# Performance work log

Hardware: AMD Instinct MI355X
Metric: run time of the kernel (lower is better)

## Reference

```python
import jax, jax.numpy as jnp
import numpy as np

D_MODEL = 768
N_HEADS = 12
D_K = D_MODEL // N_HEADS
NEG = -1e9


def setup_inputs() -> dict:
    key = jax.random.key(0)
    ks = jax.random.split(key, 10)
    B, S = 2, 2048
    x = jax.random.normal(ks[0], (B, S, D_MODEL), dtype=jnp.float32)
    # causal mask, broadcastable over batch and heads
    mask = jnp.tril(jnp.ones((S, S), dtype=jnp.int32))[None, None]
    scale = 1.0 / np.sqrt(D_MODEL)
    def lin(k):
        return jax.random.normal(k, (D_MODEL, D_MODEL), dtype=jnp.float32) * scale
    return {
        "x": x, "mask": mask,
        "wq": lin(ks[1]), "bq": jnp.zeros((D_MODEL,), jnp.float32),
        "wk": lin(ks[2]), "bk": jnp.zeros((D_MODEL,), jnp.float32),
        "wv": lin(ks[3]), "bv": jnp.zeros((D_MODEL,), jnp.float32),
        "wo": lin(ks[4]), "bo": jnp.zeros((D_MODEL,), jnp.float32),
    }


def reference(x, mask, wq, bq, wk, bk, wv, bv, wo, bo):
    B, S, _ = x.shape
    def split_heads(t):  # [B,S,D] -> [B,H,S,dk]
        return t.reshape(B, S, N_HEADS, D_K).transpose(0, 2, 1, 3)
    q = split_heads(x @ wq + bq)
    k = split_heads(x @ wk + bk)
    v = split_heads(x @ wv + bv)
    scores = jnp.einsum("bhqd,bhkd->bhqk", q, k) / jnp.sqrt(jnp.float32(D_K))
    scores = jnp.where(mask == 0, NEG, scores)
    attn = jax.nn.softmax(scores, axis=-1)
    # dropout is identity in eval mode
    ctx = jnp.einsum("bhqk,bhkd->bhqd", attn, v)
    ctx = ctx.transpose(0, 2, 1, 3).reshape(B, S, D_MODEL)
    return ctx @ wo + bo
```

## Files before the change

### kernel.cpp

```cpp
#include <hip/hip_runtime.h>
#include <hip/hip_bf16.h>
#include <stdint.h>

#define DM   768
#define NH   12
#define DKH  64
#define BB   2
#define SS   2048
#define MT   (BB*SS)
#define NQKV (3*DM)

typedef __attribute__((ext_vector_type(8))) short short8;
typedef __attribute__((ext_vector_type(4))) float f32x4;

__device__ __forceinline__ unsigned short f2bf(float f) {
    union { float f; unsigned u; } v; v.f = f;
    unsigned r = v.u + 0x7fffu + ((v.u >> 16) & 1u);
    return (unsigned short)(r >> 16);
}

__device__ __forceinline__ void gload_lds16(const unsigned short* g, unsigned short* l) {
    __builtin_amdgcn_global_load_lds((const __attribute__((address_space(1))) void*)g,
                                     (__attribute__((address_space(3))) void*)l, 16, 0, 0);
}

__global__ void k_conv_x(const float* __restrict__ x, unsigned short* __restrict__ xb) {
    int i = blockIdx.x * 256 + threadIdx.x;
    const float4 v = ((const float4*)x)[i];
    ushort4 o;
    o.x = f2bf(v.x); o.y = f2bf(v.y); o.z = f2bf(v.z); o.w = f2bf(v.w);
    ((ushort4*)xb)[i] = o;
}

__global__ void k_conv_w(const float* __restrict__ wq, const float* __restrict__ wk,
                         const float* __restrict__ wv, const float* __restrict__ wo,
                         unsigned short* __restrict__ wT) {
    __shared__ float tile[32][33];
    const int sel = blockIdx.z;
    const float* w = (sel == 0) ? wq : (sel == 1) ? wk : (sel == 2) ? wv : wo;
    const int k0 = blockIdx.x * 32, n0 = blockIdx.y * 32;
    const int tx = threadIdx.x, ty = threadIdx.y;
    #pragma unroll
    for (int j = 0; j < 4; j++)
        tile[ty + 8*j][tx] = w[(size_t)(k0 + ty + 8*j) * DM + n0 + tx];
    __syncthreads();
    #pragma unroll
    for (int j = 0; j < 4; j++)
        wT[(size_t)(sel*DM + n0 + ty + 8*j) * DM + k0 + tx] = f2bf(tile[tx][ty + 8*j]);
}

__launch_bounds__(256)
__global__ void k_gemm_qkv(const unsigned short* __restrict__ xb,
                           const unsigned short* __restrict__ wT,
                           const float* __restrict__ bq, const float* __restrict__ bk,
                           const float* __restrict__ bv,
                           unsigned short* __restrict__ Qb,
                           unsigned short* __restrict__ Kb,
                           unsigned short* __restrict__ Vt) {
    __shared__ __align__(16) unsigned short As[128][32];
    __shared__ __align__(16) unsigned short Bs[128][32];
    const int t = threadIdx.x;
    const int m0 = blockIdx.x * 128;
    const int n0 = blockIdx.y * 128;
    const int wid = t >> 6, lane = t & 63, q4 = lane >> 4, l16 = lane & 15;
    const int wm = (wid >> 1) * 64, wn = (wid & 1) * 64;

    const int srow = wid * 32 + (lane >> 2);
    const int koff = (lane & 3) * 8;
    const unsigned short* AgL = xb + (size_t)(m0 + srow) * DM + koff;
    const unsigned short* AgH = AgL + (size_t)16 * DM;
    const unsigned short* BgL = wT + (size_t)(n0 + srow) * DM + koff;
    const unsigned short* BgH = BgL + (size_t)16 * DM;
    unsigned short* ldsA1 = &As[wid*32][0];
    unsigned short* ldsA2 = &As[wid*32 + 16][0];
    unsigned short* ldsB1 = &Bs[wid*32][0];
    unsigned short* ldsB2 = &Bs[wid*32 + 16][0];

    f32x4 acc[4][4];
    for (int i = 0; i < 4; i++) for (int j = 0; j < 4; j++)
        acc[i][j] = (f32x4){0.f, 0.f, 0.f, 0.f};

    for (int kt = 0; kt < DM; kt += 32) {
        gload_lds16(AgL + kt, ldsA1);
        gload_lds16(AgH + kt, ldsA2);
        gload_lds16(BgL + kt, ldsB1);
        gload_lds16(BgH + kt, ldsB2);
        __syncthreads();
        short8 af[4], bf[4];
        for (int i = 0; i < 4; i++) af[i] = *(const short8*)&As[wm + i*16 + l16][q4*8];
        for (int i = 0; i < 4; i++) bf[i] = *(const short8*)&Bs[wn + i*16 + l16][q4*8];
        for (int mi = 0; mi < 4; mi++)
            for (int ni = 0; ni < 4; ni++)
                acc[mi][ni] = __builtin_amdgcn_mfma_f32_16x16x32_bf16(af[mi], bf[ni], acc[mi][ni], 0, 0, 0);
        __syncthreads();
    }

    const int sel = n0 / DM;
    const float* bias = (sel == 0) ? bq : (sel == 1) ? bk : bv;
    for (int ni = 0; ni < 4; ni++) {
        const int col = n0 + wn + ni*16 + l16;
        const int c = col - sel * DM;
        const float bsv = bias[c];
        const int h = c >> 6, d = c & 63;
        for (int mi = 0; mi < 4; mi++) {
            for (int r = 0; r < 4; r++) {
                const int row = m0 + wm + mi*16 + q4*4 + r;
                const int b = row >> 11, s = row & 2047;
                const int bh = b * NH + h;
                float v = acc[mi][ni][r] + bsv;
                if (sel == 0) {
                    Qb[(bh*SS + s)*DKH + d] = f2bf(v * 0.125f);
                } else if (sel == 1) {
                    Kb[(bh*SS + s)*DKH + d] = f2bf(v);
                } else {
                    Vt[(bh*DKH + d)*SS + s] = f2bf(v);
                }
            }
        }
    }
}

__launch_bounds__(256)
__global__ void k_attn(const unsigned short* __restrict__ Qb,
                       const unsigned short* __restrict__ Kb,
                       const unsigned short* __restrict__ Vt,
                       unsigned short* __restrict__ ctx) {
    __shared__ __align__(16) unsigned short Ks[2][64][72];
    __shared__ __align__(16) unsigned short Vs[2][64][72];
    __shared__ __align__(16) unsigned short P[4][16][68];
    const int t = threadIdx.x;
    const int wid = t >> 6, lane = t & 63, q4 = lane >> 4, l16 = lane & 15;
    const int lin = blockIdx.x;
    const int bh = lin % (BB * NH);
    const int qblk = 31 - lin / (BB * NH);
    const int b = bh / NH, h = bh - b * NH;
    const int qw = qblk * 64 + wid * 16;

    const unsigned short* Qp = Qb + (size_t)bh * SS * DKH;
    const unsigned short* Kp = Kb + (size_t)bh * SS * DKH;
    const unsigned short* Vp = Vt + (size_t)bh * DKH * SS;

    const int sr = t >> 3;
    const int sc = (t & 7) * 8;

    short8 qf[2];
    for (int kc = 0; kc < 2; kc++)
        qf[kc] = *(const short8*)(Qp + (qw + l16)*DKH + kc*32 + q4*8);

    f32x4 accO[4];
    for (int j = 0; j < 4; j++) accO[j] = (f32x4){0.f, 0.f, 0.f, 0.f};
    float lacc[4] = {0.f, 0.f, 0.f, 0.f};

    {
        uint4 k0 = *(const uint4*)(Kp + (size_t)(sr)      * DKH + sc);
        uint4 k1 = *(const uint4*)(Kp + (size_t)(sr + 32) * DKH + sc);
        uint4 v0 = *(const uint4*)(Vp + (size_t)(sr)      * SS  + sc);
        uint4 v1 = *(const uint4*)(Vp + (size_t)(sr + 32) * SS  + sc);
        *(uint4*)&Ks[0][sr][sc]      = k0;
        *(uint4*)&Ks[0][sr + 32][sc] = k1;
        *(uint4*)&Vs[0][sr][sc]      = v0;
        *(uint4*)&Vs[0][sr + 32][sc] = v1;
    }
    __syncthreads();

    for (int kt = 0; kt <= qblk; kt++) {
        const int cb = kt & 1, nb = cb ^ 1;
        const bool hasN = (kt < qblk);
        uint4 nk0, nk1, nv0, nv1;
        if (hasN) {
            const int kn = (kt + 1) * 64;
            nk0 = *(const uint4*)(Kp + (size_t)(kn + sr)      * DKH + sc);
            nk1 = *(const uint4*)(Kp + (size_t)(kn + sr + 32) * DKH + sc);
            nv0 = *(const uint4*)(Vp + (size_t)(sr)      * SS + kn + sc);
            nv1 = *(const uint4*)(Vp + (size_t)(sr + 32) * SS + kn + sc);
        }
        short8 kf[4][2];
        #pragma unroll
        for (int ni = 0; ni < 4; ni++)
            #pragma unroll
            for (int kc = 0; kc < 2; kc++)
                kf[ni][kc] = *(const short8*)&Ks[cb][ni*16 + l16][kc*32 + q4*8];
        f32x4 S[4];
        #pragma unroll
        for (int j = 0; j < 4; j++) S[j] = (f32x4){0.f, 0.f, 0.f, 0.f};
        #pragma unroll
        for (int ni = 0; ni < 4; ni++) {
            S[ni] = __builtin_amdgcn_mfma_f32_16x16x32_bf16(qf[0], kf[ni][0], S[ni], 0, 0, 0);
            S[ni] = __builtin_amdgcn_mfma_f32_16x16x32_bf16(qf[1], kf[ni][1], S[ni], 0, 0, 0);
        }
        if (kt == qblk) {
            #pragma unroll
            for (int ni = 0; ni < 4; ni++) {
                const int pr = q4*4, pc = ni*16 + l16;
                if (ni > wid) {
                    P[wid][pr+0][pc] = 0; P[wid][pr+1][pc] = 0;
                    P[wid][pr+2][pc] = 0; P[wid][pr+3][pc] = 0;
                    continue;
                }
                float p[4];
                if (ni == wid) {
                    #pragma unroll
                    for (int r = 0; r < 4; r++) {
                        const int qrow = qw + q4*4 + r;
                        const int key = qblk*64 + ni*16 + l16;
                        p[r] = (key > qrow) ? 0.f : __expf(S[ni][r]);
                        lacc[r] += p[r];
                    }
                } else {
                    #pragma unroll
                    for (int r = 0; r < 4; r++) {
                        p[r] = __expf(S[ni][r]);
                        lacc[r] += p[r];
                    }
                }
                union { __hip_bfloat162 v; unsigned u; } u01, u23;
                u01.v = __float22bfloat162_rn(make_float2(p[0], p[1]));
                u23.v = __float22bfloat162_rn(make_float2(p[2], p[3]));
                P[wid][pr+0][pc] = (unsigned short)(u01.u & 0xffffu);
                P[wid][pr+1][pc] = (unsigned short)(u01.u >> 16);
                P[wid][pr+2][pc] = (unsigned short)(u23.u & 0xffffu);
                P[wid][pr+3][pc] = (unsigned short)(u23.u >> 16);
            }
        } else {
            #pragma unroll
            for (int ni = 0; ni < 4; ni++) {
                float p[4];
                #pragma unroll
                for (int r = 0; r < 4; r++) {
                    p[r] = __expf(S[ni][r]);
                    lacc[r] += p[r];
                }
                union { __hip_bfloat162 v; unsigned u; } u01, u23;
                u01.v = __float22bfloat162_rn(make_float2(p[0], p[1]));
                u23.v = __float22bfloat162_rn(make_float2(p[2], p[3]));
                const int pr = q4*4, pc = ni*16 + l16;
                P[wid][pr+0][pc] = (unsigned short)(u01.u & 0xffffu);
                P[wid][pr+1][pc] = (unsigned short)(u01.u >> 16);
                P[wid][pr+2][pc] = (unsigned short)(u23.u & 0xffffu);
                P[wid][pr+3][pc] = (unsigned short)(u23.u >> 16);
            }
        }
        asm volatile("s_waitcnt lgkmcnt(0)" ::: "memory");
        short8 pf[2];
        #pragma unroll
        for (int kc = 0; kc < 2; kc++)
            pf[kc] = *(const short8*)&P[wid][l16][kc*32 + q4*8];
        short8 vf[4][2];
        #pragma unroll
        for (int ndi = 0; ndi < 4; ndi++)
            #pragma unroll
            for (int kc = 0; kc < 2; kc++)
                vf[ndi][kc] = *(const short8*)&Vs[cb][ndi*16 + l16][kc*32 + q4*8];
        #pragma unroll
        for (int ndi = 0; ndi < 4; ndi++)
            #pragma unroll
            for (int kc = 0; kc < 2; kc++)
                accO[ndi] = __builtin_amdgcn_mfma_f32_16x16x32_bf16(pf[kc], vf[ndi][kc], accO[ndi], 0, 0, 0);
        if (hasN) {
            *(uint4*)&Ks[nb][sr][sc]      = nk0;
            *(uint4*)&Ks[nb][sr + 32][sc] = nk1;
            *(uint4*)&Vs[nb][sr][sc]      = nv0;
            *(uint4*)&Vs[nb][sr + 32][sc] = nv1;
        }
        __syncthreads();
    }

    for (int r = 0; r < 4; r++) {
        float l = lacc[r];
        for (int off = 1; off < 16; off <<= 1) l += __shfl_xor(l, off);
        const float inv = 1.0f / l;
        const int s = qw + q4*4 + r;
        for (int ni = 0; ni < 4; ni++)
            ctx[((size_t)(b*SS + s))*DM + h*64 + ni*16 + l16] = f2bf(accO[ni][r] * inv);
    }
}

__launch_bounds__(256)
__global__ void k_gemm_proj(const unsigned short* __restrict__ ctx,
                            const unsigned short* __restrict__ woT,
                            const float* __restrict__ bo,
                            float* __restrict__ out) {
    __shared__ __align__(16) unsigned short As[128][32];
    __shared__ __align__(16) unsigned short Bs[64][32];
    const int t = threadIdx.x;
    const int m0 = blockIdx.x * 128;
    const int n0 = blockIdx.y * 64;
    const int wid = t >> 6, lane = t & 63, q4 = lane >> 4, l16 = lane & 15;
    const int wm = (wid >> 1) * 64, wn = (wid & 1) * 32;

    const int srowA = wid * 32 + (lane >> 2);
    const int srowB = wid * 16 + (lane >> 2);
    const int koff = (lane & 3) * 8;
    const unsigned short* AgL = ctx + (size_t)(m0 + srowA) * DM + koff;
    const unsigned short* AgH = AgL + (size_t)16 * DM;
    const unsigned short* BgL = woT + (size_t)(n0 + srowB) * DM + koff;
    unsigned short* ldsA1 = &As[wid*32][0];
    unsigned short* ldsA2 = &As[wid*32 + 16][0];
    unsigned short* ldsB1 = &Bs[wid*16][0];

    f32x4 acc[4][2];
    for (int i = 0; i < 4; i++) for (int j = 0; j < 2; j++)
        acc[i][j] = (f32x4){0.f, 0.f, 0.f, 0.f};

    for (int kt = 0; kt < DM; kt += 32) {
        gload_lds16(AgL + kt, ldsA1);
        gload_lds16(AgH + kt, ldsA2);
        gload_lds16(BgL + kt, ldsB1);
        __syncthreads();
        short8 af[4], bf[2];
        for (int i = 0; i < 4; i++) af[i] = *(const short8*)&As[wm + i*16 + l16][q4*8];
        for (int i = 0; i < 2; i++) bf[i] = *(const short8*)&Bs[wn + i*16 + l16][q4*8];
        for (int mi = 0; mi < 4; mi++)
            for (int ni = 0; ni < 2; ni++)
                acc[mi][ni] = __builtin_amdgcn_mfma_f32_16x16x32_bf16(af[mi], bf[ni], acc[mi][ni], 0, 0, 0);
        __syncthreads();
    }

    for (int ni = 0; ni < 2; ni++) {
        const int col = n0 + wn + ni*16 + l16;
        const float bsv = bo[col];
        for (int mi = 0; mi < 4; mi++) {
            for (int r = 0; r < 4; r++) {
                const int row = m0 + wm + mi*16 + q4*4 + r;
                out[(size_t)row * DM + col] = acc[mi][ni][r] + bsv;
            }
        }
    }
}

extern "C" void kernel_launch(void* const* d_in, const int* in_sizes, int n_in,
                              void* d_out, int out_size, void* d_ws, size_t ws_size,
                              hipStream_t stream) {
    const float* x  = (const float*)d_in[0];
    const float* wq = (const float*)d_in[2];
    const float* bq = (const float*)d_in[3];
    const float* wk = (const float*)d_in[4];
    const float* bk = (const float*)d_in[5];
    const float* wv = (const float*)d_in[6];
    const float* bv = (const float*)d_in[7];
    const float* wo = (const float*)d_in[8];
    const float* bo = (const float*)d_in[9];
    float* out = (float*)d_out;

    unsigned short* xb  = (unsigned short*)d_ws;
    unsigned short* wT  = xb + (size_t)MT * DM;
    unsigned short* Qb  = wT + (size_t)4 * DM * DM;
    unsigned short* Kb  = Qb + (size_t)BB * NH * SS * DKH;
    unsigned short* Vt  = Kb + (size_t)BB * NH * SS * DKH;
    unsigned short* ctx = Vt + (size_t)BB * NH * SS * DKH;

    k_conv_x<<<(MT * DM / 4) / 256, 256, 0, stream>>>(x, xb);
    k_conv_w<<<dim3(DM/32, DM/32, 4), dim3(32, 8), 0, stream>>>(wq, wk, wv, wo, wT);
    dim3 g1(MT / 128, NQKV / 128);
    k_gemm_qkv<<<g1, 256, 0, stream>>>(xb, wT, bq, bk, bv, Qb, Kb, Vt);
    k_attn<<<dim3(32 * BB * NH), 256, 0, stream>>>(Qb, Kb, Vt, ctx);
    dim3 g3(MT / 128, DM / 64);
    k_gemm_proj<<<g3, 256, 0, stream>>>(ctx, wT + (size_t)3 * DM * DM, bo, out);
}
```

Baseline: 179.6 us.

## Split long causal query blocks across two workgroups and merge partial results

The attention kernel now splits the KV range for the 16 longest query blocks per head into two halves handled by separate workgroups. Each half writes unnormalized fp32 partial outputs and row sums, and a new merge kernel combines them into ctx. Because the kernel uses no running max, the partials can simply be added. This balances the causal triangle's work across more blocks, at the cost of an extra launch and fp32 partial traffic. The x and weight conversion kernels are also fused into one launch.

```diff
diff --git a/kernel.cpp b/kernel.cpp
--- a/kernel.cpp
+++ b/kernel.cpp
@@ -24,29 +24,35 @@
                                      (__attribute__((address_space(3))) void*)l, 16, 0, 0);
 }
 
-__global__ void k_conv_x(const float* __restrict__ x, unsigned short* __restrict__ xb) {
-    int i = blockIdx.x * 256 + threadIdx.x;
-    const float4 v = ((const float4*)x)[i];
-    ushort4 o;
-    o.x = f2bf(v.x); o.y = f2bf(v.y); o.z = f2bf(v.z); o.w = f2bf(v.w);
-    ((ushort4*)xb)[i] = o;
-}
-
-__global__ void k_conv_w(const float* __restrict__ wq, const float* __restrict__ wk,
-                         const float* __restrict__ wv, const float* __restrict__ wo,
-                         unsigned short* __restrict__ wT) {
+__launch_bounds__(256)
+__global__ void k_conv(const float* __restrict__ x, unsigned short* __restrict__ xb,
+                       const float* __restrict__ wq, const float* __restrict__ wk,
+                       const float* __restrict__ wv, const float* __restrict__ wo,
+                       unsigned short* __restrict__ wT) {
     __shared__ float tile[32][33];
-    const int sel = blockIdx.z;
-    const float* w = (sel == 0) ? wq : (sel == 1) ? wk : (sel == 2) ? wv : wo;
-    const int k0 = blockIdx.x * 32, n0 = blockIdx.y * 32;
-    const int tx = threadIdx.x, ty = threadIdx.y;
-    #pragma unroll
-    for (int j = 0; j < 4; j++)
-        tile[ty + 8*j][tx] = w[(size_t)(k0 + ty + 8*j) * DM + n0 + tx];
-    __syncthreads();
-    #pragma unroll
-    for (int j = 0; j < 4; j++)
-        wT[(size_t)(sel*DM + n0 + ty + 8*j) * DM + k0 + tx] = f2bf(tile[tx][ty + 8*j]);
+    const int t = threadIdx.x;
+    if (blockIdx.x < 3072) {
+        int i = blockIdx.x * 256 + t;
+        const float4 v = ((const float4*)x)[i];
+        ushort4 o;
+        o.x = f2bf(v.x); o.y = f2bf(v.y); o.z = f2bf(v.z); o.w = f2bf(v.w);
+        ((ushort4*)xb)[i] = o;
+    } else {
+        const int cid = blockIdx.x - 3072;
+        const int sel = cid / 576;
+        const int rem = cid - sel * 576;
+        const int kb = rem / 24, nb = rem - (rem / 24) * 24;
+        const float* w = (sel == 0) ? wq : (sel == 1) ? wk : (sel == 2) ? wv : wo;
+        const int k0 = kb * 32, n0 = nb * 32;
+        const int tx = t & 31, ty = t >> 5;
+        #pragma unroll
+        for (int j = 0; j < 4; j++)
+            tile[ty + 8*j][tx] = w[(size_t)(k0 + ty + 8*j) * DM + n0 + tx];
+        __syncthreads();
+        #pragma unroll
+        for (int j = 0; j < 4; j++)
+            wT[(size_t)(sel*DM + n0 + ty + 8*j) * DM + k0 + tx] = f2bf(tile[tx][ty + 8*j]);
+    }
 }
 
 __launch_bounds__(256)
@@ -124,7 +130,8 @@
 __global__ void k_attn(const unsigned short* __restrict__ Qb,
                        const unsigned short* __restrict__ Kb,
                        const unsigned short* __restrict__ Vt,
-                       unsigned short* __restrict__ ctx) {
+                       unsigned short* __restrict__ ctx,
+                       float* __restrict__ Op, float* __restrict__ Lp) {
     __shared__ __align__(16) unsigned short Ks[2][64][72];
     __shared__ __align__(16) unsigned short Vs[2][64][72];
     __shared__ __align__(16) unsigned short P[4][16][68];
@@ -132,7 +139,21 @@
     const int wid = t >> 6, lane = t & 63, q4 = lane >> 4, l16 = lane & 15;
     const int lin = blockIdx.x;
     const int bh = lin % (BB * NH);
-    const int qblk = 31 - lin / (BB * NH);
+    const int j = lin / (BB * NH);
+    int qblk, k0, k1, half;
+    bool split;
+    if (j < 32) {
+        split = true;
+        qblk = 31 - (j >> 1);
+        half = j & 1;
+        const int n = qblk + 1, nh = n >> 1;
+        k0 = half ? nh : 0;
+        k1 = half ? n : nh;
+    } else {
+        split = false; half = 0;
+        qblk = 47 - j;
+        k0 = 0; k1 = qblk + 1;
+    }
     const int b = bh / NH, h = bh - b * NH;
     const int qw = qblk * 64 + wid * 16;
 
@@ -148,24 +169,25 @@
         qf[kc] = *(const short8*)(Qp + (qw + l16)*DKH + kc*32 + q4*8);
 
     f32x4 accO[4];
-    for (int j = 0; j < 4; j++) accO[j] = (f32x4){0.f, 0.f, 0.f, 0.f};
+    for (int jj = 0; jj < 4; jj++) accO[jj] = (f32x4){0.f, 0.f, 0.f, 0.f};
     float lacc[4] = {0.f, 0.f, 0.f, 0.f};
 
     {
-        uint4 k0 = *(const uint4*)(Kp + (size_t)(sr)      * DKH + sc);
-        uint4 k1 = *(const uint4*)(Kp + (size_t)(sr + 32) * DKH + sc);
-        uint4 v0 = *(const uint4*)(Vp + (size_t)(sr)      * SS  + sc);
-        uint4 v1 = *(const uint4*)(Vp + (size_t)(sr + 32) * SS  + sc);
-        *(uint4*)&Ks[0][sr][sc]      = k0;
-        *(uint4*)&Ks[0][sr + 32][sc] = k1;
-        *(uint4*)&Vs[0][sr][sc]      = v0;
-        *(uint4*)&Vs[0][sr + 32][sc] = v1;
+        const int kb0 = k0 * 64;
+        uint4 ka = *(const uint4*)(Kp + (size_t)(kb0 + sr)      * DKH + sc);
+        uint4 kb = *(const uint4*)(Kp + (size_t)(kb0 + sr + 32) * DKH + sc);
+        uint4 va = *(const uint4*)(Vp + (size_t)(sr)      * SS + kb0 + sc);
+        uint4 vb = *(const uint4*)(Vp + (size_t)(sr + 32) * SS + kb0 + sc);
+        *(uint4*)&Ks[0][sr][sc]      = ka;
+        *(uint4*)&Ks[0][sr + 32][sc] = kb;
+        *(uint4*)&Vs[0][sr][sc]      = va;
+        *(uint4*)&Vs[0][sr + 32][sc] = vb;
     }
     __syncthreads();
 
-    for (int kt = 0; kt <= qblk; kt++) {
-        const int cb = kt & 1, nb = cb ^ 1;
-        const bool hasN = (kt < qblk);
+    for (int kt = k0; kt < k1; kt++) {
+        const int cb = (kt - k0) & 1, nb = cb ^ 1;
+        const bool hasN = (kt + 1 < k1);
         uint4 nk0, nk1, nv0, nv1;
         if (hasN) {
             const int kn = (kt + 1) * 64;
@@ -182,7 +204,7 @@
                 kf[ni][kc] = *(const short8*)&Ks[cb][ni*16 + l16][kc*32 + q4*8];
         f32x4 S[4];
         #pragma unroll
-        for (int j = 0; j < 4; j++) S[j] = (f32x4){0.f, 0.f, 0.f, 0.f};
+        for (int jj = 0; jj < 4; jj++) S[jj] = (f32x4){0.f, 0.f, 0.f, 0.f};
         #pragma unroll
         for (int ni = 0; ni < 4; ni++) {
             S[ni] = __builtin_amdgcn_mfma_f32_16x16x32_bf16(qf[0], kf[ni][0], S[ni], 0, 0, 0);
@@ -208,10 +230,7 @@
                     }
                 } else {
                     #pragma unroll
-                    for (int r = 0; r < 4; r++) {
-                        p[r] = __expf(S[ni][r]);
-                        lacc[r] += p[r];
-                    }
+                    for (int r = 0; r < 4; r++) { p[r] = __expf(S[ni][r]); lacc[r] += p[r]; }
                 }
                 union { __hip_bfloat162 v; unsigned u; } u01, u23;
                 u01.v = __float22bfloat162_rn(make_float2(p[0], p[1]));
@@ -226,10 +245,7 @@
             for (int ni = 0; ni < 4; ni++) {
                 float p[4];
                 #pragma unroll
-                for (int r = 0; r < 4; r++) {
-                    p[r] = __expf(S[ni][r]);
-                    lacc[r] += p[r];
-                }
+                for (int r = 0; r < 4; r++) { p[r] = __expf(S[ni][r]); lacc[r] += p[r]; }
                 union { __hip_bfloat162 v; unsigned u; } u01, u23;
                 u01.v = __float22bfloat162_rn(make_float2(p[0], p[1]));
                 u23.v = __float22bfloat162_rn(make_float2(p[2], p[3]));
@@ -265,14 +281,44 @@
         __syncthreads();
     }
 
-    for (int r = 0; r < 4; r++) {
-        float l = lacc[r];
-        for (int off = 1; off < 16; off <<= 1) l += __shfl_xor(l, off);
-        const float inv = 1.0f / l;
-        const int s = qw + q4*4 + r;
-        for (int ni = 0; ni < 4; ni++)
-            ctx[((size_t)(b*SS + s))*DM + h*64 + ni*16 + l16] = f2bf(accO[ni][r] * inv);
-    }
+    if (!split) {
+        for (int r = 0; r < 4; r++) {
+            float l = lacc[r];
+            for (int off = 1; off < 16; off <<= 1) l += __shfl_xor(l, off);
+            const float inv = 1.0f / l;
+            const int s = qw + q4*4 + r;
+            for (int ni = 0; ni < 4; ni++)
+                ctx[((size_t)(b*SS + s))*DM + h*64 + ni*16 + l16] = f2bf(accO[ni][r] * inv);
+        }
+    } else {
+        const size_t e = ((size_t)(bh*16 + (qblk - 16)) * 2 + half);
+        float* Od = Op + e * 64 * 64;
+        for (int r = 0; r < 4; r++) {
+            float l = lacc[r];
+            for (int off = 1; off < 16; off <<= 1) l += __shfl_xor(l, off);
+            const int row = wid*16 + q4*4 + r;
+            if (l16 == 0) Lp[e*64 + row] = l;
+            for (int ni = 0; ni < 4; ni++)
+                Od[row*64 + ni*16 + l16] = accO[ni][r];
+        }
+    }
+}
+
+__launch_bounds__(256)
+__global__ void k_merge(const float* __restrict__ Op, const float* __restrict__ Lp,
+                        unsigned short* __restrict__ ctx) {
+    const int idx = blockIdx.x * 256 + threadIdx.x;
+    const int col = idx & 63;
+    const int row = (idx >> 6) & 63;
+    const int qb  = (idx >> 12) & 15;
+    const int bh  = idx >> 16;
+    const size_t e0 = ((size_t)(bh*16 + qb) * 2) * 4096;
+    const float O = Op[e0 + row*64 + col] + Op[e0 + 4096 + row*64 + col];
+    const size_t le = ((size_t)(bh*16 + qb) * 2) * 64;
+    const float l = Lp[le + row] + Lp[le + 64 + row];
+    const int b = bh / NH, h = bh - b * NH;
+    const int s = (qb + 16) * 64 + row;
+    ctx[((size_t)(b*SS + s))*DM + h*64 + col] = f2bf(O / l);
 }
 
 __launch_bounds__(256)
@@ -348,12 +394,14 @@
     unsigned short* Kb  = Qb + (size_t)BB * NH * SS * DKH;
     unsigned short* Vt  = Kb + (size_t)BB * NH * SS * DKH;
     unsigned short* ctx = Vt + (size_t)BB * NH * SS * DKH;
-
-    k_conv_x<<<(MT * DM / 4) / 256, 256, 0, stream>>>(x, xb);
-    k_conv_w<<<dim3(DM/32, DM/32, 4), dim3(32, 8), 0, stream>>>(wq, wk, wv, wo, wT);
+    float* Op = (float*)(ctx + (size_t)MT * DM);
+    float* Lp = Op + (size_t)24 * 16 * 2 * 4096;
+
+    k_conv<<<3072 + 2304, 256, 0, stream>>>(x, xb, wq, wk, wv, wo, wT);
     dim3 g1(MT / 128, NQKV / 128);
     k_gemm_qkv<<<g1, 256, 0, stream>>>(xb, wT, bq, bk, bv, Qb, Kb, Vt);
-    k_attn<<<dim3(32 * BB * NH), 256, 0, stream>>>(Qb, Kb, Vt, ctx);
+    k_attn<<<dim3(48 * BB * NH), 256, 0, stream>>>(Qb, Kb, Vt, ctx, Op, Lp);
+    k_merge<<<(24*16*64*64) / 256, 256, 0, stream>>>(Op, Lp, ctx);
     dim3 g3(MT / 128, DM / 64);
     k_gemm_proj<<<g3, 256, 0, stream>>>(ctx, wT + (size_t)3 * DM * DM, bo, out);
 }
```

Measured after the change: 183.0 us. Within noise of the previous version (+1.9%).
